# Kernel tuning notes

Hardware: AMD Instinct MI355X
Metric: run time of the kernel (lower is better)

Reference implementation:

```python
import jax, jax.numpy as jnp
import numpy as np

HIDDEN = 20
VOCAB = 29
NUM_LAYERS = 1
SEQ_LEN = 64
BATCH = 16384


def setup_inputs() -> dict:
    key = jax.random.key(0)
    k1, k2, k3, k4, k5 = jax.random.split(key, 5)
    return {
        "x": jax.random.normal(k1, (SEQ_LEN, BATCH, VOCAB), dtype=jnp.float32),
        "img_emb": jax.random.normal(k2, (BATCH, HIDDEN), dtype=jnp.float32),
        "W_ih": jax.random.normal(k3, (NUM_LAYERS, HIDDEN, VOCAB), dtype=jnp.float32),
        "b_ih": jnp.zeros((NUM_LAYERS, HIDDEN), dtype=jnp.float32),
        "W_hh": jax.random.normal(k4, (NUM_LAYERS, HIDDEN, HIDDEN), dtype=jnp.float32),
        "b_hh": jnp.zeros((NUM_LAYERS, HIDDEN), dtype=jnp.float32),
        "W_ho": jax.random.normal(k5, (VOCAB, HIDDEN), dtype=jnp.float32),
        "b_ho": jnp.zeros((VOCAB,), dtype=jnp.float32),
    }


def reference(x, img_emb, W_ih, b_ih, W_hh, b_hh, W_ho, b_ho):
    # num_layers == 1: take layer 0 weights
    Wi, bi = W_ih[0], b_ih[0]   # [H,V], [H]
    Wh, bh = W_hh[0], b_hh[0]   # [H,H], [H]
    seq_len, batch = x.shape[0], x.shape[1]
    # img_emb is only added at t == 0
    first = (jnp.arange(seq_len) == 0).astype(x.dtype)  # [T]

    def step(h, inp):
        xt, f = inp  # xt: [B,V], f: scalar
        h_new = jnp.tanh(xt @ Wi.T + bi + h @ Wh.T + bh + f * img_emb)
        return h_new, h_new

    h0 = jnp.zeros((batch, Wi.shape[0]), dtype=x.dtype)
    _, hs = jax.lax.scan(step, h0, (x, first))  # hs: [T,B,H]
    logits = hs @ W_ho.T + b_ho  # [T,B,V]
    return jax.nn.log_softmax(logits, axis=-1)
```

## Files before the change

kernel.cpp:

```cpp
#include <hip/hip_runtime.h>

#define Tn 64
#define Bn 16384
#define Vn 29
#define Hn 20

typedef float f4 __attribute__((ext_vector_type(4)));

static __device__ __forceinline__ f4 ld4u(const float* p) {
  f4 v; __builtin_memcpy(&v, p, 16); return v;
}
static __device__ __forceinline__ void st4u(float* p, f4 v) {
  __builtin_memcpy(p, &v, 16);
}

#define LOG2E 1.4426950408889634f
#define LN2   0.6931471805599453f

static __device__ __forceinline__ float frcp(float x) {
#if __has_builtin(__builtin_amdgcn_rcpf)
  return __builtin_amdgcn_rcpf(x);
#else
  return 1.0f / x;
#endif
}
static __device__ __forceinline__ float fexp2(float x) {
#if __has_builtin(__builtin_amdgcn_exp2f)
  return __builtin_amdgcn_exp2f(x);
#else
  return exp2f(x);
#endif
}
static __device__ __forceinline__ float flog2(float x) {
#if __has_builtin(__builtin_amdgcn_logf)
  return __builtin_amdgcn_logf(x);
#else
  return log2f(x);
#endif
}
static __device__ __forceinline__ float ftanh(float x) {
  float e = fexp2(x * (2.0f * LOG2E));
  return 1.0f - 2.0f * frcp(1.0f + e);
}

#define SWZ(v, imm) __int_as_float(__builtin_amdgcn_ds_swizzle(__float_as_int(v), (imm)))
#define PAT(ow) (((ow) << 5) | 0x18)

#if __has_builtin(__builtin_amdgcn_update_dpp)
#define DPPF(v, ctrl) __int_as_float(__builtin_amdgcn_update_dpp( \
    0, __float_as_int(v), (ctrl), 0xF, 0xF, true))
#define DPP_XOR1(v) DPPF(v, 0xB1)
#define DPP_XOR2(v) DPPF(v, 0x4E)
#else
#define DPP_XOR1(v) SWZ(v, 0x041F)
#define DPP_XOR2(v) SWZ(v, 0x081F)
#endif

#define XI_STEP(xv, c) { \
  float xb_ = SWZ((xv)[(c) & 3], PAT((c) >> 2)); \
  a0 += wi0[(c)] * xb_; a1 += wi1[(c)] * xb_; a2 += wi2[(c)] * xb_; }

#define XI_ALL(xv) \
  XI_STEP(xv, 0)  XI_STEP(xv, 1)  XI_STEP(xv, 2)  XI_STEP(xv, 3)  \
  XI_STEP(xv, 4)  XI_STEP(xv, 5)  XI_STEP(xv, 6)  XI_STEP(xv, 7)  \
  XI_STEP(xv, 8)  XI_STEP(xv, 9)  XI_STEP(xv, 10) XI_STEP(xv, 11) \
  XI_STEP(xv, 12) XI_STEP(xv, 13) XI_STEP(xv, 14) XI_STEP(xv, 15) \
  XI_STEP(xv, 16) XI_STEP(xv, 17) XI_STEP(xv, 18) XI_STEP(xv, 19) \
  XI_STEP(xv, 20) XI_STEP(xv, 21) XI_STEP(xv, 22) XI_STEP(xv, 23) \
  XI_STEP(xv, 24) XI_STEP(xv, 25) XI_STEP(xv, 26) XI_STEP(xv, 27) \
  XI_STEP(xv, 28)

static __device__ __forceinline__ f4 ldx(const float* row, int j) {
  f4 v;
  if (j < 7) v = ld4u(row + 4 * j);
  else       v = f4{row[28], 0.0f, 0.0f, 0.0f};
  return v;
}

__global__ __attribute__((amdgpu_waves_per_eu(1, 1))) __launch_bounds__(256)
void k_fused(
    const float* __restrict__ x,   const float* __restrict__ img,
    const float* __restrict__ Wi,  const float* __restrict__ bi,
    const float* __restrict__ Wh,  const float* __restrict__ bh,
    const float* __restrict__ Who, const float* __restrict__ bho,
    float* __restrict__ out)
{
  const int gt = blockIdx.x * 256 + threadIdx.x;
  const int b = gt >> 3;
  const int j = gt & 7;

  int r0 = 3 * j;     r0 = r0 > 19 ? 19 : r0;
  int r1 = 3 * j + 1; r1 = r1 > 19 ? 19 : r1;
  int r2 = 3 * j + 2; r2 = r2 > 19 ? 19 : r2;

  float wi0[Vn], wi1[Vn], wi2[Vn];
#pragma unroll
  for (int q = 0; q < 7; ++q) {
    f4 a = ld4u(Wi + r0 * Vn + 4 * q);
    f4 c = ld4u(Wi + r1 * Vn + 4 * q);
    f4 d = ld4u(Wi + r2 * Vn + 4 * q);
    wi0[4*q]=a.x; wi0[4*q+1]=a.y; wi0[4*q+2]=a.z; wi0[4*q+3]=a.w;
    wi1[4*q]=c.x; wi1[4*q+1]=c.y; wi1[4*q+2]=c.z; wi1[4*q+3]=c.w;
    wi2[4*q]=d.x; wi2[4*q+1]=d.y; wi2[4*q+2]=d.z; wi2[4*q+3]=d.w;
  }
  wi0[28] = Wi[r0 * Vn + 28];
  wi1[28] = Wi[r1 * Vn + 28];
  wi2[28] = Wi[r2 * Vn + 28];

  float wh0[Hn], wh1[Hn], wh2[Hn];
#pragma unroll
  for (int q = 0; q < 5; ++q) {
    f4 a = *(const f4*)(Wh + r0 * Hn + 4 * q);
    f4 c = *(const f4*)(Wh + r1 * Hn + 4 * q);
    f4 d = *(const f4*)(Wh + r2 * Hn + 4 * q);
    wh0[4*q]=a.x; wh0[4*q+1]=a.y; wh0[4*q+2]=a.z; wh0[4*q+3]=a.w;
    wh1[4*q]=c.x; wh1[4*q+1]=c.y; wh1[4*q+2]=c.z; wh1[4*q+3]=c.w;
    wh2[4*q]=d.x; wh2[4*q+1]=d.y; wh2[4*q+2]=d.z; wh2[4*q+3]=d.w;
  }

  float wo[4][Hn], bo[4];
#pragma unroll
  for (int rr = 0; rr < 4; ++rr) {
    int v = 4 * j + rr; int vc = v > 28 ? 28 : v;
#pragma unroll
    for (int q = 0; q < 5; ++q) {
      f4 w = *(const f4*)(Who + vc * Hn + 4 * q);
      wo[rr][4*q]=w.x; wo[rr][4*q+1]=w.y; wo[rr][4*q+2]=w.z; wo[rr][4*q+3]=w.w;
    }
    bo[rr] = (v < Vn) ? bho[v] : -1e30f;
  }

  const float bs0 = bi[r0] + bh[r0];
  const float bs1 = bi[r1] + bh[r1];
  const float bs2 = bi[r2] + bh[r2];

  const size_t S = (size_t)Bn * Vn;
  const float* xrow = x + (size_t)b * Vn;

  f4 xv = ldx(xrow, j);
  f4 xA = ldx(xrow + S, j);
  f4 xB = ldx(xrow + 2 * S, j);
  const float* pf = xrow + 3 * S;

  float a0 = 0.0f, a1 = 0.0f, a2 = 0.0f;
  XI_ALL(xv)
  a0 += bs0 + img[(size_t)b * Hn + r0];
  a1 += bs1 + img[(size_t)b * Hn + r1];
  a2 += bs2 + img[(size_t)b * Hn + r2];

  float hbc[Hn];
#pragma unroll
  for (int k = 0; k < Hn; ++k) hbc[k] = 0.0f;

  float* op = out + (size_t)b * Vn + 4 * j;
  const size_t ostep = (size_t)Bn * Vn;

#pragma unroll 1
  for (int t = 0; t < Tn; ++t) {
    f4 xC = ldx(pf, j);
    if (t < 60) pf += S;

    float A0 = a0, A1 = a1, A2 = a2;
#pragma unroll
    for (int k = 0; k < Hn; ++k) {
      float hk = hbc[k];
      A0 += hk * wh0[k]; A1 += hk * wh1[k]; A2 += hk * wh2[k];
    }
    float h0 = ftanh(A0), h1 = ftanh(A1), h2 = ftanh(A2);

    hbc[0]  = SWZ(h0, PAT(0)); hbc[1]  = SWZ(h1, PAT(0)); hbc[2]  = SWZ(h2, PAT(0));
    hbc[3]  = SWZ(h0, PAT(1)); hbc[4]  = SWZ(h1, PAT(1)); hbc[5]  = SWZ(h2, PAT(1));
    hbc[6]  = SWZ(h0, PAT(2)); hbc[7]  = SWZ(h1, PAT(2)); hbc[8]  = SWZ(h2, PAT(2));
    hbc[9]  = SWZ(h0, PAT(3)); hbc[10] = SWZ(h1, PAT(3)); hbc[11] = SWZ(h2, PAT(3));
    hbc[12] = SWZ(h0, PAT(4)); hbc[13] = SWZ(h1, PAT(4)); hbc[14] = SWZ(h2, PAT(4));
    hbc[15] = SWZ(h0, PAT(5)); hbc[16] = SWZ(h1, PAT(5)); hbc[17] = SWZ(h2, PAT(5));
    hbc[18] = SWZ(h0, PAT(6)); hbc[19] = SWZ(h1, PAT(6));

    float l0 = bo[0], l1 = bo[1], l2 = bo[2], l3 = bo[3];
#pragma unroll
    for (int k = 0; k < Hn; ++k) {
      float hk = hbc[k];
      l0 += hk * wo[0][k]; l1 += hk * wo[1][k];
      l2 += hk * wo[2][k]; l3 += hk * wo[3][k];
    }

    float m = fmaxf(fmaxf(l0, l1), fmaxf(l2, l3));
    m = fmaxf(m, DPP_XOR1(m));
    m = fmaxf(m, DPP_XOR2(m));
    m = fmaxf(m, SWZ(m, 0x101F));
    float e0 = fexp2((l0 - m) * LOG2E), e1 = fexp2((l1 - m) * LOG2E);
    float e2 = fexp2((l2 - m) * LOG2E), e3 = fexp2((l3 - m) * LOG2E);
    float s = e0 + e1 + e2 + e3;
    s += DPP_XOR1(s);
    s += DPP_XOR2(s);
    s += SWZ(s, 0x101F);
    float ls = m + flog2(s) * LN2;

    f4 o = f4{l0 - ls, l1 - ls, l2 - ls, l3 - ls};
    if (j < 7) st4u(op, o);
    else       op[0] = l0 - ls;
    op += ostep;

    a0 = 0.0f; a1 = 0.0f; a2 = 0.0f;
    XI_ALL(xA)
    a0 += bs0; a1 += bs1; a2 += bs2;

    xA = xB; xB = xC;
  }
}

extern "C" void kernel_launch(void* const* d_in, const int* in_sizes, int n_in,
                              void* d_out, int out_size, void* d_ws, size_t ws_size,
                              hipStream_t stream)
{
  const float* x   = (const float*)d_in[0];
  const float* img = (const float*)d_in[1];
  const float* Wi  = (const float*)d_in[2];
  const float* bi  = (const float*)d_in[3];
  const float* Wh  = (const float*)d_in[4];
  const float* bh  = (const float*)d_in[5];
  const float* Who = (const float*)d_in[6];
  const float* bho = (const float*)d_in[7];
  float* out = (float*)d_out;

  k_fused<<<(8 * Bn) / 256, 256, 0, stream>>>(x, img, Wi, bi, Wh, bh, Who, bho, out);
}
```

Baseline: 378.5 us.

## Split fused RNN into recurrence kernel and separate output/log-softmax kernel

Splits the single fused kernel into two. The first runs the recurrence with 16 lanes per batch row, two hidden units per lane, and writes the hidden states to workspace. The second computes logits and log-softmax over all timesteps in parallel, with grid-stride prefetch. This moves the output projection off the serial recurrence path and raises parallelism. The cost is an extra global round trip for the hidden states (T*B*H floats) and a second kernel launch.

```diff
diff --git a/kernel.cpp b/kernel.cpp
--- a/kernel.cpp
+++ b/kernel.cpp
@@ -6,9 +6,13 @@
 #define Hn 20
 
 typedef float f4 __attribute__((ext_vector_type(4)));
+typedef float f2 __attribute__((ext_vector_type(2)));
 
 static __device__ __forceinline__ f4 ld4u(const float* p) {
   f4 v; __builtin_memcpy(&v, p, 16); return v;
+}
+static __device__ __forceinline__ f2 ld2u(const float* p) {
+  f2 v; __builtin_memcpy(&v, p, 8); return v;
 }
 static __device__ __forceinline__ void st4u(float* p, f4 v) {
   __builtin_memcpy(p, &v, 16);
@@ -44,7 +48,8 @@
 }
 
 #define SWZ(v, imm) __int_as_float(__builtin_amdgcn_ds_swizzle(__float_as_int(v), (imm)))
-#define PAT(ow) (((ow) << 5) | 0x18)
+#define P16(ow) (((ow) << 5) | 0x10)
+#define P8(ow)  (((ow) << 5) | 0x18)
 
 #if __has_builtin(__builtin_amdgcn_update_dpp)
 #define DPPF(v, ctrl) __int_as_float(__builtin_amdgcn_update_dpp( \
@@ -56,133 +61,184 @@
 #define DPP_XOR2(v) SWZ(v, 0x081F)
 #endif
 
-#define XI_STEP(xv, c) { \
-  float xb_ = SWZ((xv)[(c) & 3], PAT((c) >> 2)); \
-  a0 += wi0[(c)] * xb_; a1 += wi1[(c)] * xb_; a2 += wi2[(c)] * xb_; }
-
-#define XI_ALL(xv) \
-  XI_STEP(xv, 0)  XI_STEP(xv, 1)  XI_STEP(xv, 2)  XI_STEP(xv, 3)  \
-  XI_STEP(xv, 4)  XI_STEP(xv, 5)  XI_STEP(xv, 6)  XI_STEP(xv, 7)  \
-  XI_STEP(xv, 8)  XI_STEP(xv, 9)  XI_STEP(xv, 10) XI_STEP(xv, 11) \
-  XI_STEP(xv, 12) XI_STEP(xv, 13) XI_STEP(xv, 14) XI_STEP(xv, 15) \
-  XI_STEP(xv, 16) XI_STEP(xv, 17) XI_STEP(xv, 18) XI_STEP(xv, 19) \
-  XI_STEP(xv, 20) XI_STEP(xv, 21) XI_STEP(xv, 22) XI_STEP(xv, 23) \
-  XI_STEP(xv, 24) XI_STEP(xv, 25) XI_STEP(xv, 26) XI_STEP(xv, 27) \
-  XI_STEP(xv, 28)
-
-static __device__ __forceinline__ f4 ldx(const float* row, int j) {
-  f4 v;
-  if (j < 7) v = ld4u(row + 4 * j);
-  else       v = f4{row[28], 0.0f, 0.0f, 0.0f};
+
+#define XIA_STEP(c) { \
+  float xb_ = SWZ(((c) & 1) ? xN1.y : xN1.x, P16((c) >> 1)); \
+  aA += wiA[(c)] * xb_; aB += wiB[(c)] * xb_; }
+#define XIA_ALL \
+  XIA_STEP(0)  XIA_STEP(1)  XIA_STEP(2)  XIA_STEP(3)  XIA_STEP(4)  \
+  XIA_STEP(5)  XIA_STEP(6)  XIA_STEP(7)  XIA_STEP(8)  XIA_STEP(9)  \
+  XIA_STEP(10) XIA_STEP(11) XIA_STEP(12) XIA_STEP(13) XIA_STEP(14) \
+  XIA_STEP(15) XIA_STEP(16) XIA_STEP(17) XIA_STEP(18) XIA_STEP(19) \
+  XIA_STEP(20) XIA_STEP(21) XIA_STEP(22) XIA_STEP(23) XIA_STEP(24) \
+  XIA_STEP(25) XIA_STEP(26) XIA_STEP(27) XIA_STEP(28)
+
+#define XI0_STEP(c) { \
+  float xb_ = SWZ(((c) & 1) ? xv.y : xv.x, P16((c) >> 1)); \
+  aA += wiA[(c)] * xb_; aB += wiB[(c)] * xb_; }
+#define XI0_ALL \
+  XI0_STEP(0)  XI0_STEP(1)  XI0_STEP(2)  XI0_STEP(3)  XI0_STEP(4)  \
+  XI0_STEP(5)  XI0_STEP(6)  XI0_STEP(7)  XI0_STEP(8)  XI0_STEP(9)  \
+  XI0_STEP(10) XI0_STEP(11) XI0_STEP(12) XI0_STEP(13) XI0_STEP(14) \
+  XI0_STEP(15) XI0_STEP(16) XI0_STEP(17) XI0_STEP(18) XI0_STEP(19) \
+  XI0_STEP(20) XI0_STEP(21) XI0_STEP(22) XI0_STEP(23) XI0_STEP(24) \
+  XI0_STEP(25) XI0_STEP(26) XI0_STEP(27) XI0_STEP(28)
+
+#define WH_STEP(k) { \
+  float hk_ = SWZ(((k) < 16) ? hA : hB, P16(((k) < 16) ? (k) : ((k) - 16))); \
+  aA += hk_ * whA[(k)]; aB += hk_ * whB[(k)]; }
+#define WH_ALL \
+  WH_STEP(0)  WH_STEP(1)  WH_STEP(2)  WH_STEP(3)  WH_STEP(4)  \
+  WH_STEP(5)  WH_STEP(6)  WH_STEP(7)  WH_STEP(8)  WH_STEP(9)  \
+  WH_STEP(10) WH_STEP(11) WH_STEP(12) WH_STEP(13) WH_STEP(14) \
+  WH_STEP(15) WH_STEP(16) WH_STEP(17) WH_STEP(18) WH_STEP(19)
+
+static __device__ __forceinline__ f2 ldx16(const float* row, int j) {
+  f2 v;
+  if (j < 14)      v = ld2u(row + 2 * j);
+  else if (j == 14) v = f2{row[28], 0.0f};
+  else              v = f2{0.0f, 0.0f};
   return v;
 }
 
-__global__ __attribute__((amdgpu_waves_per_eu(1, 1))) __launch_bounds__(256)
-void k_fused(
-    const float* __restrict__ x,   const float* __restrict__ img,
-    const float* __restrict__ Wi,  const float* __restrict__ bi,
-    const float* __restrict__ Wh,  const float* __restrict__ bh,
-    const float* __restrict__ Who, const float* __restrict__ bho,
-    float* __restrict__ out)
+__global__ __launch_bounds__(256) void k_rec(
+    const float* __restrict__ x,  const float* __restrict__ img,
+    const float* __restrict__ Wi, const float* __restrict__ bi,
+    const float* __restrict__ Wh, const float* __restrict__ bh,
+    float* __restrict__ hs)
 {
   const int gt = blockIdx.x * 256 + threadIdx.x;
-  const int b = gt >> 3;
-  const int j = gt & 7;
-
-  int r0 = 3 * j;     r0 = r0 > 19 ? 19 : r0;
-  int r1 = 3 * j + 1; r1 = r1 > 19 ? 19 : r1;
-  int r2 = 3 * j + 2; r2 = r2 > 19 ? 19 : r2;
-
-  float wi0[Vn], wi1[Vn], wi2[Vn];
+  const int b = gt >> 4;
+  const int j = gt & 15;
+
+  const int rA = j;
+  const int rB = (j < 4) ? (j + 16) : 19;
+
+  float wiA[Vn], wiB[Vn];
 #pragma unroll
   for (int q = 0; q < 7; ++q) {
-    f4 a = ld4u(Wi + r0 * Vn + 4 * q);
-    f4 c = ld4u(Wi + r1 * Vn + 4 * q);
-    f4 d = ld4u(Wi + r2 * Vn + 4 * q);
-    wi0[4*q]=a.x; wi0[4*q+1]=a.y; wi0[4*q+2]=a.z; wi0[4*q+3]=a.w;
-    wi1[4*q]=c.x; wi1[4*q+1]=c.y; wi1[4*q+2]=c.z; wi1[4*q+3]=c.w;
-    wi2[4*q]=d.x; wi2[4*q+1]=d.y; wi2[4*q+2]=d.z; wi2[4*q+3]=d.w;
-  }
-  wi0[28] = Wi[r0 * Vn + 28];
-  wi1[28] = Wi[r1 * Vn + 28];
-  wi2[28] = Wi[r2 * Vn + 28];
-
-  float wh0[Hn], wh1[Hn], wh2[Hn];
+    f4 a = ld4u(Wi + rA * Vn + 4 * q);
+    f4 c = ld4u(Wi + rB * Vn + 4 * q);
+    wiA[4*q]=a.x; wiA[4*q+1]=a.y; wiA[4*q+2]=a.z; wiA[4*q+3]=a.w;
+    wiB[4*q]=c.x; wiB[4*q+1]=c.y; wiB[4*q+2]=c.z; wiB[4*q+3]=c.w;
+  }
+  wiA[28] = Wi[rA * Vn + 28];
+  wiB[28] = Wi[rB * Vn + 28];
+
+  float whA[Hn], whB[Hn];
 #pragma unroll
   for (int q = 0; q < 5; ++q) {
-    f4 a = *(const f4*)(Wh + r0 * Hn + 4 * q);
-    f4 c = *(const f4*)(Wh + r1 * Hn + 4 * q);
-    f4 d = *(const f4*)(Wh + r2 * Hn + 4 * q);
-    wh0[4*q]=a.x; wh0[4*q+1]=a.y; wh0[4*q+2]=a.z; wh0[4*q+3]=a.w;
-    wh1[4*q]=c.x; wh1[4*q+1]=c.y; wh1[4*q+2]=c.z; wh1[4*q+3]=c.w;
-    wh2[4*q]=d.x; wh2[4*q+1]=d.y; wh2[4*q+2]=d.z; wh2[4*q+3]=d.w;
-  }
-
-  float wo[4][Hn], bo[4];
-#pragma unroll
-  for (int rr = 0; rr < 4; ++rr) {
-    int v = 4 * j + rr; int vc = v > 28 ? 28 : v;
+    f4 a = *(const f4*)(Wh + rA * Hn + 4 * q);
+    f4 c = *(const f4*)(Wh + rB * Hn + 4 * q);
+    whA[4*q]=a.x; whA[4*q+1]=a.y; whA[4*q+2]=a.z; whA[4*q+3]=a.w;
+    whB[4*q]=c.x; whB[4*q+1]=c.y; whB[4*q+2]=c.z; whB[4*q+3]=c.w;
+  }
+
+  const float bsA = bi[rA] + bh[rA];
+  const float bsB = bi[rB] + bh[rB];
+
+  const size_t S = (size_t)Bn * Vn;
+  const float* xrow = x + (size_t)b * Vn;
+
+  f2 xv  = ldx16(xrow, j);
+  f2 xN1 = ldx16(xrow + S, j);
+  f2 xN2 = ldx16(xrow + 2 * S, j);
+  const float* pf = xrow + 3 * S;
+
+  float aA = bsA + img[(size_t)b * Hn + rA];
+  float aB = bsB + img[(size_t)b * Hn + rB];
+  XI0_ALL
+
+  float hA = 0.0f, hB = 0.0f;
+
+  float* hp = hs + (size_t)b * Hn;
+  const size_t hstep = (size_t)Bn * Hn;
+
+#pragma unroll 1
+  for (int t = 0; t < Tn; ++t) {
+    f2 xC = ldx16(pf, j);
+    if (t < 60) pf += S;
+
+    WH_ALL
+    hA = ftanh(aA);
+    hB = ftanh(aB);
+
+    hp[rA] = hA;
+    if (j < 4) hp[16 + j] = hB;
+    hp += hstep;
+
+    aA = bsA; aB = bsB;
+    XIA_ALL
+    xN1 = xN2; xN2 = xC;
+  }
+  (void)xv;
+}
+
+
+#define OWN(k) ((k) >= 18 ? 6 : (k) / 3)
+#define HSEL(k) (((k) - 3 * OWN(k)) == 0 ? hl0 : (((k) - 3 * OWN(k)) == 1 ? hl1 : hl2))
+#define LG_STEP(k) { \
+  float hk_ = SWZ(HSEL(k), P8(OWN(k))); \
+  l0 += hk_ * wo0[(k)]; l1 += hk_ * wo1[(k)]; \
+  l2 += hk_ * wo2[(k)]; l3 += hk_ * wo3[(k)]; }
+#define LG_ALL \
+  LG_STEP(0)  LG_STEP(1)  LG_STEP(2)  LG_STEP(3)  LG_STEP(4)  \
+  LG_STEP(5)  LG_STEP(6)  LG_STEP(7)  LG_STEP(8)  LG_STEP(9)  \
+  LG_STEP(10) LG_STEP(11) LG_STEP(12) LG_STEP(13) LG_STEP(14) \
+  LG_STEP(15) LG_STEP(16) LG_STEP(17) LG_STEP(18) LG_STEP(19)
+
+#define OUT_ITERS 8
+
+__global__ __launch_bounds__(256) void k_out(
+    const float* __restrict__ hs, const float* __restrict__ Who,
+    const float* __restrict__ bho, float* __restrict__ out)
+{
+  const int gt = blockIdx.x * 256 + threadIdx.x;
+  const int g = gt >> 3;
+  const int j = gt & 7;
+  const int NG = (gridDim.x * 256) >> 3;
+
+  float wo0[Hn], wo1[Hn], wo2[Hn], wo3[Hn];
+  float bo0, bo1, bo2, bo3;
+  {
+    int v0 = 4 * j, v1 = 4 * j + 1, v2 = 4 * j + 2, v3 = 4 * j + 3;
+    int c0v = v0 > 28 ? 28 : v0, c1v = v1 > 28 ? 28 : v1;
+    int c2v = v2 > 28 ? 28 : v2, c3v = v3 > 28 ? 28 : v3;
 #pragma unroll
     for (int q = 0; q < 5; ++q) {
-      f4 w = *(const f4*)(Who + vc * Hn + 4 * q);
-      wo[rr][4*q]=w.x; wo[rr][4*q+1]=w.y; wo[rr][4*q+2]=w.z; wo[rr][4*q+3]=w.w;
+      f4 w0 = *(const f4*)(Who + c0v * Hn + 4 * q);
+      f4 w1 = *(const f4*)(Who + c1v * Hn + 4 * q);
+      f4 w2 = *(const f4*)(Who + c2v * Hn + 4 * q);
+      f4 w3 = *(const f4*)(Who + c3v * Hn + 4 * q);
+      wo0[4*q]=w0.x; wo0[4*q+1]=w0.y; wo0[4*q+2]=w0.z; wo0[4*q+3]=w0.w;
+      wo1[4*q]=w1.x; wo1[4*q+1]=w1.y; wo1[4*q+2]=w1.z; wo1[4*q+3]=w1.w;
+      wo2[4*q]=w2.x; wo2[4*q+1]=w2.y; wo2[4*q+2]=w2.z; wo2[4*q+3]=w2.w;
+      wo3[4*q]=w3.x; wo3[4*q+1]=w3.y; wo3[4*q+2]=w3.z; wo3[4*q+3]=w3.w;
     }
-    bo[rr] = (v < Vn) ? bho[v] : -1e30f;
-  }
-
-  const float bs0 = bi[r0] + bh[r0];
-  const float bs1 = bi[r1] + bh[r1];
-  const float bs2 = bi[r2] + bh[r2];
-
-  const size_t S = (size_t)Bn * Vn;
-  const float* xrow = x + (size_t)b * Vn;
-
-  f4 xv = ldx(xrow, j);
-  f4 xA = ldx(xrow + S, j);
-  f4 xB = ldx(xrow + 2 * S, j);
-  const float* pf = xrow + 3 * S;
-
-  float a0 = 0.0f, a1 = 0.0f, a2 = 0.0f;
-  XI_ALL(xv)
-  a0 += bs0 + img[(size_t)b * Hn + r0];
-  a1 += bs1 + img[(size_t)b * Hn + r1];
-  a2 += bs2 + img[(size_t)b * Hn + r2];
-
-  float hbc[Hn];
-#pragma unroll
-  for (int k = 0; k < Hn; ++k) hbc[k] = 0.0f;
-
-  float* op = out + (size_t)b * Vn + 4 * j;
-  const size_t ostep = (size_t)Bn * Vn;
+    bo0 = (v0 < Vn) ? bho[v0] : -1e30f;
+    bo1 = (v1 < Vn) ? bho[v1] : -1e30f;
+    bo2 = (v2 < Vn) ? bho[v2] : -1e30f;
+    bo3 = (v3 < Vn) ? bho[v3] : -1e30f;
+  }
+
+  int c0 = 3 * j;     c0 = c0 > 19 ? 19 : c0;
+  int c1 = 3 * j + 1; c1 = c1 > 19 ? 19 : c1;
+  int c2 = 3 * j + 2; c2 = c2 > 19 ? 19 : c2;
+
+  size_t e = (size_t)g;
+  const float* hp = hs + e * Hn;
+  float hl0 = hp[c0], hl1 = hp[c1], hl2 = hp[c2];
 
 #pragma unroll 1
-  for (int t = 0; t < Tn; ++t) {
-    f4 xC = ldx(pf, j);
-    if (t < 60) pf += S;
-
-    float A0 = a0, A1 = a1, A2 = a2;
-#pragma unroll
-    for (int k = 0; k < Hn; ++k) {
-      float hk = hbc[k];
-      A0 += hk * wh0[k]; A1 += hk * wh1[k]; A2 += hk * wh2[k];
+  for (int it = 0; it < OUT_ITERS; ++it) {
+    float nl0 = 0.0f, nl1 = 0.0f, nl2 = 0.0f;
+    if (it + 1 < OUT_ITERS) {
+      const float* np = hs + (e + NG) * Hn;
+      nl0 = np[c0]; nl1 = np[c1]; nl2 = np[c2];
     }
-    float h0 = ftanh(A0), h1 = ftanh(A1), h2 = ftanh(A2);
-
-    hbc[0]  = SWZ(h0, PAT(0)); hbc[1]  = SWZ(h1, PAT(0)); hbc[2]  = SWZ(h2, PAT(0));
-    hbc[3]  = SWZ(h0, PAT(1)); hbc[4]  = SWZ(h1, PAT(1)); hbc[5]  = SWZ(h2, PAT(1));
-    hbc[6]  = SWZ(h0, PAT(2)); hbc[7]  = SWZ(h1, PAT(2)); hbc[8]  = SWZ(h2, PAT(2));
-    hbc[9]  = SWZ(h0, PAT(3)); hbc[10] = SWZ(h1, PAT(3)); hbc[11] = SWZ(h2, PAT(3));
-    hbc[12] = SWZ(h0, PAT(4)); hbc[13] = SWZ(h1, PAT(4)); hbc[14] = SWZ(h2, PAT(4));
-    hbc[15] = SWZ(h0, PAT(5)); hbc[16] = SWZ(h1, PAT(5)); hbc[17] = SWZ(h2, PAT(5));
-    hbc[18] = SWZ(h0, PAT(6)); hbc[19] = SWZ(h1, PAT(6));
-
-    float l0 = bo[0], l1 = bo[1], l2 = bo[2], l3 = bo[3];
-#pragma unroll
-    for (int k = 0; k < Hn; ++k) {
-      float hk = hbc[k];
-      l0 += hk * wo[0][k]; l1 += hk * wo[1][k];
-      l2 += hk * wo[2][k]; l3 += hk * wo[3][k];
-    }
+
+    float l0 = bo0, l1 = bo1, l2 = bo2, l3 = bo3;
+    LG_ALL
 
     float m = fmaxf(fmaxf(l0, l1), fmaxf(l2, l3));
     m = fmaxf(m, DPP_XOR1(m));
@@ -196,16 +252,13 @@
     s += SWZ(s, 0x101F);
     float ls = m + flog2(s) * LN2;
 
+    float* op = out + e * Vn + 4 * j;
     f4 o = f4{l0 - ls, l1 - ls, l2 - ls, l3 - ls};
     if (j < 7) st4u(op, o);
     else       op[0] = l0 - ls;
-    op += ostep;
-
-    a0 = 0.0f; a1 = 0.0f; a2 = 0.0f;
-    XI_ALL(xA)
-    a0 += bs0; a1 += bs1; a2 += bs2;
-
-    xA = xB; xB = xC;
+
+    hl0 = nl0; hl1 = nl1; hl2 = nl2;
+    e += NG;
   }
 }
 
@@ -222,6 +275,8 @@
   const float* Who = (const float*)d_in[6];
   const float* bho = (const float*)d_in[7];
   float* out = (float*)d_out;
-
-  k_fused<<<(8 * Bn) / 256, 256, 0, stream>>>(x, img, Wi, bi, Wh, bh, Who, bho, out);
-}
+  float* hws = (float*)d_ws;
+
+  k_rec<<<(16 * Bn) / 256, 256, 0, stream>>>(x, img, Wi, bi, Wh, bh, hws);
+  k_out<<<(Tn * Bn * 8 / OUT_ITERS) / 256, 256, 0, stream>>>(hws, Who, bho, out);
+}
```

Result: slower. 397.3 us (+5.0%).
